# Kernel tuning notes

Hardware: AMD Instinct MI355X
Metric: run time of the kernel (lower is better)

## Reference

```python
import jax, jax.numpy as jnp
import numpy as np
from jax import lax

B, N, F_IN, T = 4, 30000, 2, 12
HID, HORIZON, E = 32, 12, 240000


def setup_inputs() -> dict:
    key = jax.random.key(0)
    ks = jax.random.split(key, 20)

    def lin_init(k, fan_in, shape):
        b = 1.0 / np.sqrt(fan_in)
        return jax.random.uniform(k, shape, jnp.float32, -b, b)

    def glorot(k, shape):
        b = np.sqrt(6.0 / (shape[0] + shape[1]))
        return jax.random.uniform(k, shape, jnp.float32, -b, b)

    return {
        "x": jax.random.normal(ks[0], (B, N, F_IN, T), jnp.float32),
        "edge_index": jax.random.randint(ks[1], (2, E), 0, N, jnp.int32),
        # A3TGCN2 attention over periods (init: uniform[0,1))
        "attention": jax.random.uniform(ks[2], (T,), jnp.float32),
        # TGCN2 gates: GCNConv weight (F_IN,HID) + bias, Linear (2*HID,HID) + bias
        "conv_z_w": glorot(ks[3], (F_IN, HID)), "conv_z_b": jnp.zeros((HID,), jnp.float32),
        "lin_z_w": lin_init(ks[4], 2 * HID, (2 * HID, HID)), "lin_z_b": lin_init(ks[5], 2 * HID, (HID,)),
        "conv_r_w": glorot(ks[6], (F_IN, HID)), "conv_r_b": jnp.zeros((HID,), jnp.float32),
        "lin_r_w": lin_init(ks[7], 2 * HID, (2 * HID, HID)), "lin_r_b": lin_init(ks[8], 2 * HID, (HID,)),
        "conv_h_w": glorot(ks[9], (F_IN, HID)), "conv_h_b": jnp.zeros((HID,), jnp.float32),
        "lin_h_w": lin_init(ks[10], 2 * HID, (2 * HID, HID)), "lin_h_b": lin_init(ks[11], 2 * HID, (HID,)),
        # trailing head Linear(HID, HORIZON)
        "head_w": lin_init(ks[12], HID, (HID, HORIZON)), "head_b": lin_init(ks[13], HID, (HORIZON,)),
    }


def _forward(x, attention, conv_z_w, conv_z_b, lin_z_w, lin_z_b,
             conv_r_w, conv_r_b, lin_r_w, lin_r_b,
             conv_h_w, conv_h_b, lin_h_w, lin_h_b,
             head_w, head_b, edge_index):
    b, n = x.shape[0], x.shape[1]
    # GCN normalization with added self loops: D^-1/2 (A+I) D^-1/2
    loop = jnp.arange(n, dtype=edge_index.dtype)
    src = jnp.concatenate([edge_index[0], loop])  # (E+N,) message sources
    dst = jnp.concatenate([edge_index[1], loop])  # (E+N,) message targets
    deg = jnp.zeros((n,), x.dtype).at[dst].add(1.0)  # deg >= 1 due to self loops
    dinv = lax.rsqrt(deg)
    norm = dinv[src] * dinv[dst]  # (E+N,)

    def gcn(xt, W, bias):
        # xt: (B,N,F) -> (B,N,HID); gather from src, scatter-add to dst
        xw = jnp.einsum('bnf,fh->bnh', xt, W)
        msg = xw[:, src, :] * norm[None, :, None]  # (B,E+N,HID)
        agg = jnp.zeros((b, n, W.shape[1]), xt.dtype).at[:, dst, :].add(msg)
        return agg + bias

    probs = jax.nn.softmax(attention)  # (T,)
    H0 = jnp.zeros((b, n, HID), x.dtype)  # A3TGCN2 passes H=None every period

    def step(acc, inps):
        xt, p = inps  # xt: (B,N,F)
        Z = jax.nn.sigmoid(jnp.concatenate([gcn(xt, conv_z_w, conv_z_b), H0], -1) @ lin_z_w + lin_z_b)
        R = jax.nn.sigmoid(jnp.concatenate([gcn(xt, conv_r_w, conv_r_b), H0], -1) @ lin_r_w + lin_r_b)
        Ht = jnp.tanh(jnp.concatenate([gcn(xt, conv_h_w, conv_h_b), H0 * R], -1) @ lin_h_w + lin_h_b)
        Hn = Z * H0 + (1.0 - Z) * Ht
        return acc + p * Hn, None

    acc, _ = lax.scan(step, H0, (jnp.moveaxis(x, 3, 0), probs))
    return jax.nn.relu(acc) @ head_w + head_b  # (B,N,HORIZON)


def reference(x, edge_index, attention, conv_z_w, conv_z_b, lin_z_w, lin_z_b,
              conv_r_w, conv_r_b, lin_r_w, lin_r_b,
              conv_h_w, conv_h_b, lin_h_w, lin_h_b, head_w, head_b):
    return _forward(x, attention, conv_z_w, conv_z_b, lin_z_w, lin_z_b,
                    conv_r_w, conv_r_b, lin_r_w, lin_r_b,
                    conv_h_w, conv_h_b, lin_h_w, lin_h_b,
                    head_w, head_b, edge_index)
```

## Files before the change

kernel.cpp:

```cpp
#include <hip/hip_runtime.h>

#define BB   4
#define NN   30000
#define TT   12
#define EE   240000
#define FT   24
#define NM   96
#define CAP  32
#define OVCAP 2048
#define FB   ((EE + 255) / 256)
#define LOG2E 1.44269504088896340736f

#define WS_CNT 0
#define WS_OVC 30000
#define WS_EFF 30016
#define WS_OVF 30272
#define WS_BKT 34368

__device__ __forceinline__ float readlane_f(float v, int l) {
    return __int_as_float(__builtin_amdgcn_readlane(__float_as_int(v), l));
}

__global__ void __launch_bounds__(256)
k_pre(const int* __restrict__ src, const int* __restrict__ dst,
      const float* __restrict__ czw, const float* __restrict__ czb,
      const float* __restrict__ lzw, const float* __restrict__ lzb,
      const float* __restrict__ chw, const float* __restrict__ chb,
      const float* __restrict__ lhw, const float* __restrict__ lhb,
      const float* __restrict__ att,
      int* __restrict__ cnt, int* __restrict__ ovc,
      int* __restrict__ ovf, int* __restrict__ bucket, float* __restrict__ eff) {
    int bid = blockIdx.x, lt = threadIdx.x;
    if (bid < FB) {
        int e = bid * 256 + lt;
        if (e < EE) {
            int d = dst[e], s = src[e];
            int slot = atomicAdd(&cnt[d], 1);
            if (slot < CAP) {
                bucket[d * CAP + slot] = s;
            } else {
                int o = atomicAdd(ovc, 1);
                if (o < OVCAP) { ovf[2 * o] = d; ovf[2 * o + 1] = s; }
            }
        }
        return;
    }
    int j = lt;
    if (j < 32) {
        float wz0 = 0.f, wz1 = 0.f, bz = 0.f, wh0 = 0.f, wh1 = 0.f, bh = 0.f;
        for (int k = 0; k < 32; ++k) {
            float lz = lzw[k * 32 + j], lh = lhw[k * 32 + j];
            wz0 = fmaf(czw[k],      lz, wz0);
            wz1 = fmaf(czw[32 + k], lz, wz1);
            bz  = fmaf(czb[k],      lz, bz);
            wh0 = fmaf(chw[k],      lh, wh0);
            wh1 = fmaf(chw[32 + k], lh, wh1);
            bh  = fmaf(chb[k],      lh, bh);
        }
        eff[j]        = -LOG2E * wz0;
        eff[32 + j]   = -LOG2E * wz1;
        eff[64 + j]   = -LOG2E * (bz + lzb[j]);
        eff[96 + j]   = 2.0f * LOG2E * wh0;
        eff[128 + j]  = 2.0f * LOG2E * wh1;
        eff[160 + j]  = 2.0f * LOG2E * (bh + lhb[j]);
    } else if (j == 32) {
        float m = -1e30f;
        for (int t = 0; t < TT; ++t) m = fmaxf(m, att[t]);
        float p[TT], s = 0.f;
        for (int t = 0; t < TT; ++t) { p[t] = __expf(att[t] - m); s += p[t]; }
        float inv = 1.0f / s;
        for (int t = 0; t < TT; ++t) eff[192 + t] = p[t] * inv;
    }
}

__global__ void __launch_bounds__(256)
k_fused(const float* __restrict__ x, const int* __restrict__ cnt,
        const int* __restrict__ ovc, const int* __restrict__ ovf,
        const int* __restrict__ bucket, const float* __restrict__ eff,
        const float* __restrict__ hw, const float* __restrict__ hb,
        float* __restrict__ out) {
    __shared__ float se[204];
    __shared__ float shwT[384];
    __shared__ float shb[12];
    __shared__ float sx[4 * NM];
    __shared__ float lacc[4 * 128];
    const int lt = threadIdx.x, lane = lt & 63, w = lt >> 6;
    const int n = blockIdx.x * 4 + w;

    if (lt < 204) se[lt] = eff[lt];
    if (lt < 12) shb[lt] = hb[lt];
    for (int i = lt; i < 384; i += 256) {
        int jj = i / 12, kk = i - 12 * jj;
        shwT[kk * 32 + jj] = hw[i];
    }
    __syncthreads();

    const bool act = (lane < 48);
    const int b = lane / 12, f2 = lane - 12 * b;
    const float2* xb = (const float2*)x;
    const int lane_off = b * (NN * 12) + f2;

    const int deg = __builtin_amdgcn_readfirstlane(cnt[n]);
    const int m = (deg < CAP) ? deg : CAP;
    int sv = (lane < m) ? bucket[n * CAP + lane] : n;
    float wv = (lane <= m) ? rsqrtf((float)(cnt[sv] + 1)) : 0.f;

    float2 acc = {0.f, 0.f};
    const int total = m + 1;
    int k = 0;
    for (; k + 8 <= total; k += 8) {
        int s0 = __builtin_amdgcn_readlane(sv, k);
        int s1 = __builtin_amdgcn_readlane(sv, k + 1);
        int s2 = __builtin_amdgcn_readlane(sv, k + 2);
        int s3 = __builtin_amdgcn_readlane(sv, k + 3);
        int s4 = __builtin_amdgcn_readlane(sv, k + 4);
        int s5 = __builtin_amdgcn_readlane(sv, k + 5);
        int s6 = __builtin_amdgcn_readlane(sv, k + 6);
        int s7 = __builtin_amdgcn_readlane(sv, k + 7);
        if (act) {
            float2 v0 = xb[lane_off + s0 * 12];
            float2 v1 = xb[lane_off + s1 * 12];
            float2 v2 = xb[lane_off + s2 * 12];
            float2 v3 = xb[lane_off + s3 * 12];
            float2 v4 = xb[lane_off + s4 * 12];
            float2 v5 = xb[lane_off + s5 * 12];
            float2 v6 = xb[lane_off + s6 * 12];
            float2 v7 = xb[lane_off + s7 * 12];
            float w0 = readlane_f(wv, k),     w1 = readlane_f(wv, k + 1);
            float w2 = readlane_f(wv, k + 2), w3 = readlane_f(wv, k + 3);
            float w4 = readlane_f(wv, k + 4), w5 = readlane_f(wv, k + 5);
            float w6 = readlane_f(wv, k + 6), w7 = readlane_f(wv, k + 7);
            acc.x = fmaf(w0, v0.x, acc.x); acc.y = fmaf(w0, v0.y, acc.y);
            acc.x = fmaf(w1, v1.x, acc.x); acc.y = fmaf(w1, v1.y, acc.y);
            acc.x = fmaf(w2, v2.x, acc.x); acc.y = fmaf(w2, v2.y, acc.y);
            acc.x = fmaf(w3, v3.x, acc.x); acc.y = fmaf(w3, v3.y, acc.y);
            acc.x = fmaf(w4, v4.x, acc.x); acc.y = fmaf(w4, v4.y, acc.y);
            acc.x = fmaf(w5, v5.x, acc.x); acc.y = fmaf(w5, v5.y, acc.y);
            acc.x = fmaf(w6, v6.x, acc.x); acc.y = fmaf(w6, v6.y, acc.y);
            acc.x = fmaf(w7, v7.x, acc.x); acc.y = fmaf(w7, v7.y, acc.y);
        }
    }
    for (; k < total; k += 4) {
        int s0 = __builtin_amdgcn_readlane(sv, k);
        int s1 = __builtin_amdgcn_readlane(sv, k + 1);
        int s2 = __builtin_amdgcn_readlane(sv, k + 2);
        int s3 = __builtin_amdgcn_readlane(sv, k + 3);
        if (act) {
            float2 v0 = xb[lane_off + s0 * 12];
            float2 v1 = xb[lane_off + s1 * 12];
            float2 v2 = xb[lane_off + s2 * 12];
            float2 v3 = xb[lane_off + s3 * 12];
            float w0 = readlane_f(wv, k),     w1 = readlane_f(wv, k + 1);
            float w2 = readlane_f(wv, k + 2), w3 = readlane_f(wv, k + 3);
            acc.x = fmaf(w0, v0.x, acc.x); acc.y = fmaf(w0, v0.y, acc.y);
            acc.x = fmaf(w1, v1.x, acc.x); acc.y = fmaf(w1, v1.y, acc.y);
            acc.x = fmaf(w2, v2.x, acc.x); acc.y = fmaf(w2, v2.y, acc.y);
            acc.x = fmaf(w3, v3.x, acc.x); acc.y = fmaf(w3, v3.y, acc.y);
        }
    }

    int nov = __builtin_amdgcn_readfirstlane(*ovc);
    if (nov > 0) {
        if (nov > OVCAP) nov = OVCAP;
        for (int i = 0; i < nov; ++i) {
            int d = ovf[2 * i];
            if (d == n) {
                int s = ovf[2 * i + 1];
                float ws_ = rsqrtf((float)(cnt[s] + 1));
                if (act) {
                    float2 v = xb[lane_off + s * 12];
                    acc.x = fmaf(ws_, v.x, acc.x);
                    acc.y = fmaf(ws_, v.y, acc.y);
                }
            }
        }
    }

    const float dn = readlane_f(wv, m);
    if (act) {
        float2* sx2 = (float2*)(sx + w * NM + b * FT);
        sx2[f2] = make_float2(dn * acc.x, dn * acc.y);
    }
    __syncthreads();

    const int j = lane & 31, b0_ = lane >> 5;
    const float az0 = se[j],      az1 = se[32 + j],  ab = se[64 + j];
    const float ch0 = se[96 + j], ch1 = se[128 + j], cb = se[160 + j];
#pragma unroll
    for (int bi = 0; bi < 2; ++bi) {
        const int bb = b0_ + 2 * bi;
        const float4* s4 = (const float4*)(sx + w * NM + bb * FT);
        float4 q[6];
#pragma unroll
        for (int i = 0; i < 6; ++i) q[i] = s4[i];
        const float* av = (const float*)q;
        float a = 0.f;
#pragma unroll
        for (int t = 0; t < TT; ++t) {
            float v0 = av[t], v1 = av[12 + t], pp = se[192 + t];
            float ae = fmaf(v1, az1, fmaf(v0, az0, ab));
            float ce = fmaf(v1, ch1, fmaf(v0, ch0, cb));
            ae = __builtin_amdgcn_fmed3f(ae, -126.f, 126.f);
            ce = __builtin_amdgcn_fmed3f(ce, -126.f, 126.f);
            float u  = __builtin_amdgcn_exp2f(ae);
            float e2 = __builtin_amdgcn_exp2f(ce);
            float t1  = 1.0f + u;
            float den = fmaf(e2, t1, t1);
            float num = fmaf(u, e2, -u);
            float r   = __builtin_amdgcn_rcpf(den);
            a = fmaf(pp * num, r, a);
        }
        lacc[w * 128 + bb * 32 + j] = fmaxf(a, 0.f);
    }
    __syncthreads();

    if (lane < 48) {
        int bb = lane / 12, kk = lane - 12 * bb;
        float r = shb[kk];
        const float4* la4 = (const float4*)(lacc + w * 128 + bb * 32);
        const float4* wt4 = (const float4*)(shwT + kk * 32);
#pragma unroll
        for (int i = 0; i < 8; ++i) {
            float4 a4 = la4[i], w4 = wt4[i];
            r = fmaf(a4.x, w4.x, r); r = fmaf(a4.y, w4.y, r);
            r = fmaf(a4.z, w4.z, r); r = fmaf(a4.w, w4.w, r);
        }
        out[((long long)bb * NN + n) * 12 + kk] = r;
    }
}

extern "C" void kernel_launch(void* const* d_in, const int* in_sizes, int n_in,
                              void* d_out, int out_size, void* d_ws, size_t ws_size,
                              hipStream_t stream) {
    const float* x   = (const float*)d_in[0];
    const int*   ei  = (const int*)d_in[1];
    const float* att = (const float*)d_in[2];
    const float* czw = (const float*)d_in[3];
    const float* czb = (const float*)d_in[4];
    const float* lzw = (const float*)d_in[5];
    const float* lzb = (const float*)d_in[6];
    const float* chw = (const float*)d_in[11];
    const float* chb = (const float*)d_in[12];
    const float* lhw = (const float*)d_in[13];
    const float* lhb = (const float*)d_in[14];
    const float* hw  = (const float*)d_in[15];
    const float* hb  = (const float*)d_in[16];
    float* out = (float*)d_out;

    float* ws = (float*)d_ws;
    int*   cnt = (int*)(ws + WS_CNT);
    int*   ovc = (int*)(ws + WS_OVC);
    float* eff = ws + WS_EFF;
    int*   ovf = (int*)(ws + WS_OVF);
    int*   bkt = (int*)(ws + WS_BKT);

    const int* src = ei;
    const int* dst = ei + EE;

    hipMemsetAsync(cnt, 0, WS_EFF * 4, stream);
    k_pre<<<FB + 1, 256, 0, stream>>>(src, dst, czw, czb, lzw, lzb,
                                      chw, chb, lhw, lhb, att,
                                      cnt, ovc, ovf, bkt, eff);
    k_fused<<<NN / 4, 256, 0, stream>>>(x, cnt, ovc, ovf, bkt, eff, hw, hb, out);
}
```

Before: 141.9 us.

## Process two nodes per wavefront with interleaved gathers and wave-level barriers

Each wavefront now handles two destination nodes, interleaving their 8-wide neighbor gathers so more independent global loads are in flight per wave. The block-wide __syncthreads are replaced by wave barriers, since each wave only touches its own shared-memory slices. Shared-memory rows are padded to a stride of 36 to reduce bank conflicts, and the grid is halved. The trade-offs are higher register pressure, fewer blocks, and the remainder loop now always issues full 8-wide gathers, reading padded lanes that carry zero weight.

```diff
diff --git a/kernel.cpp b/kernel.cpp
--- a/kernel.cpp
+++ b/kernel.cpp
@@ -73,6 +73,41 @@
     }
 }
 
+__device__ __forceinline__ void gath8(const float2* __restrict__ xb, int lane_off,
+                                      bool act, int sv, float wv, int k,
+                                      float2& acc) {
+    int s0 = __builtin_amdgcn_readlane(sv, k);
+    int s1 = __builtin_amdgcn_readlane(sv, k + 1);
+    int s2 = __builtin_amdgcn_readlane(sv, k + 2);
+    int s3 = __builtin_amdgcn_readlane(sv, k + 3);
+    int s4 = __builtin_amdgcn_readlane(sv, k + 4);
+    int s5 = __builtin_amdgcn_readlane(sv, k + 5);
+    int s6 = __builtin_amdgcn_readlane(sv, k + 6);
+    int s7 = __builtin_amdgcn_readlane(sv, k + 7);
+    if (act) {
+        float2 v0 = xb[lane_off + s0 * 12];
+        float2 v1 = xb[lane_off + s1 * 12];
+        float2 v2 = xb[lane_off + s2 * 12];
+        float2 v3 = xb[lane_off + s3 * 12];
+        float2 v4 = xb[lane_off + s4 * 12];
+        float2 v5 = xb[lane_off + s5 * 12];
+        float2 v6 = xb[lane_off + s6 * 12];
+        float2 v7 = xb[lane_off + s7 * 12];
+        float w0 = readlane_f(wv, k),     w1 = readlane_f(wv, k + 1);
+        float w2 = readlane_f(wv, k + 2), w3 = readlane_f(wv, k + 3);
+        float w4 = readlane_f(wv, k + 4), w5 = readlane_f(wv, k + 5);
+        float w6 = readlane_f(wv, k + 6), w7 = readlane_f(wv, k + 7);
+        acc.x = fmaf(w0, v0.x, acc.x); acc.y = fmaf(w0, v0.y, acc.y);
+        acc.x = fmaf(w1, v1.x, acc.x); acc.y = fmaf(w1, v1.y, acc.y);
+        acc.x = fmaf(w2, v2.x, acc.x); acc.y = fmaf(w2, v2.y, acc.y);
+        acc.x = fmaf(w3, v3.x, acc.x); acc.y = fmaf(w3, v3.y, acc.y);
+        acc.x = fmaf(w4, v4.x, acc.x); acc.y = fmaf(w4, v4.y, acc.y);
+        acc.x = fmaf(w5, v5.x, acc.x); acc.y = fmaf(w5, v5.y, acc.y);
+        acc.x = fmaf(w6, v6.x, acc.x); acc.y = fmaf(w6, v6.y, acc.y);
+        acc.x = fmaf(w7, v7.x, acc.x); acc.y = fmaf(w7, v7.y, acc.y);
+    }
+}
+
 __global__ void __launch_bounds__(256)
 k_fused(const float* __restrict__ x, const int* __restrict__ cnt,
         const int* __restrict__ ovc, const int* __restrict__ ovf,
@@ -80,18 +115,19 @@
         const float* __restrict__ hw, const float* __restrict__ hb,
         float* __restrict__ out) {
     __shared__ float se[204];
-    __shared__ float shwT[384];
+    __shared__ float shwT[432];
     __shared__ float shb[12];
-    __shared__ float sx[4 * NM];
-    __shared__ float lacc[4 * 128];
+    __shared__ float sx[8 * NM];
+    __shared__ float lacc[32 * 36];
     const int lt = threadIdx.x, lane = lt & 63, w = lt >> 6;
-    const int n = blockIdx.x * 4 + w;
+    const int n0 = blockIdx.x * 8 + w * 2;
+    const int n1 = n0 + 1;
 
     if (lt < 204) se[lt] = eff[lt];
     if (lt < 12) shb[lt] = hb[lt];
     for (int i = lt; i < 384; i += 256) {
         int jj = i / 12, kk = i - 12 * jj;
-        shwT[kk * 32 + jj] = hw[i];
+        shwT[kk * 36 + jj] = hw[i];
     }
     __syncthreads();
 
@@ -100,63 +136,21 @@
     const float2* xb = (const float2*)x;
     const int lane_off = b * (NN * 12) + f2;
 
-    const int deg = __builtin_amdgcn_readfirstlane(cnt[n]);
-    const int m = (deg < CAP) ? deg : CAP;
-    int sv = (lane < m) ? bucket[n * CAP + lane] : n;
-    float wv = (lane <= m) ? rsqrtf((float)(cnt[sv] + 1)) : 0.f;
-
-    float2 acc = {0.f, 0.f};
-    const int total = m + 1;
-    int k = 0;
-    for (; k + 8 <= total; k += 8) {
-        int s0 = __builtin_amdgcn_readlane(sv, k);
-        int s1 = __builtin_amdgcn_readlane(sv, k + 1);
-        int s2 = __builtin_amdgcn_readlane(sv, k + 2);
-        int s3 = __builtin_amdgcn_readlane(sv, k + 3);
-        int s4 = __builtin_amdgcn_readlane(sv, k + 4);
-        int s5 = __builtin_amdgcn_readlane(sv, k + 5);
-        int s6 = __builtin_amdgcn_readlane(sv, k + 6);
-        int s7 = __builtin_amdgcn_readlane(sv, k + 7);
-        if (act) {
-            float2 v0 = xb[lane_off + s0 * 12];
-            float2 v1 = xb[lane_off + s1 * 12];
-            float2 v2 = xb[lane_off + s2 * 12];
-            float2 v3 = xb[lane_off + s3 * 12];
-            float2 v4 = xb[lane_off + s4 * 12];
-            float2 v5 = xb[lane_off + s5 * 12];
-            float2 v6 = xb[lane_off + s6 * 12];
-            float2 v7 = xb[lane_off + s7 * 12];
-            float w0 = readlane_f(wv, k),     w1 = readlane_f(wv, k + 1);
-            float w2 = readlane_f(wv, k + 2), w3 = readlane_f(wv, k + 3);
-            float w4 = readlane_f(wv, k + 4), w5 = readlane_f(wv, k + 5);
-            float w6 = readlane_f(wv, k + 6), w7 = readlane_f(wv, k + 7);
-            acc.x = fmaf(w0, v0.x, acc.x); acc.y = fmaf(w0, v0.y, acc.y);
-            acc.x = fmaf(w1, v1.x, acc.x); acc.y = fmaf(w1, v1.y, acc.y);
-            acc.x = fmaf(w2, v2.x, acc.x); acc.y = fmaf(w2, v2.y, acc.y);
-            acc.x = fmaf(w3, v3.x, acc.x); acc.y = fmaf(w3, v3.y, acc.y);
-            acc.x = fmaf(w4, v4.x, acc.x); acc.y = fmaf(w4, v4.y, acc.y);
-            acc.x = fmaf(w5, v5.x, acc.x); acc.y = fmaf(w5, v5.y, acc.y);
-            acc.x = fmaf(w6, v6.x, acc.x); acc.y = fmaf(w6, v6.y, acc.y);
-            acc.x = fmaf(w7, v7.x, acc.x); acc.y = fmaf(w7, v7.y, acc.y);
-        }
-    }
-    for (; k < total; k += 4) {
-        int s0 = __builtin_amdgcn_readlane(sv, k);
-        int s1 = __builtin_amdgcn_readlane(sv, k + 1);
-        int s2 = __builtin_amdgcn_readlane(sv, k + 2);
-        int s3 = __builtin_amdgcn_readlane(sv, k + 3);
-        if (act) {
-            float2 v0 = xb[lane_off + s0 * 12];
-            float2 v1 = xb[lane_off + s1 * 12];
-            float2 v2 = xb[lane_off + s2 * 12];
-            float2 v3 = xb[lane_off + s3 * 12];
-            float w0 = readlane_f(wv, k),     w1 = readlane_f(wv, k + 1);
-            float w2 = readlane_f(wv, k + 2), w3 = readlane_f(wv, k + 3);
-            acc.x = fmaf(w0, v0.x, acc.x); acc.y = fmaf(w0, v0.y, acc.y);
-            acc.x = fmaf(w1, v1.x, acc.x); acc.y = fmaf(w1, v1.y, acc.y);
-            acc.x = fmaf(w2, v2.x, acc.x); acc.y = fmaf(w2, v2.y, acc.y);
-            acc.x = fmaf(w3, v3.x, acc.x); acc.y = fmaf(w3, v3.y, acc.y);
-        }
+    const int deg0 = __builtin_amdgcn_readfirstlane(cnt[n0]);
+    const int deg1 = __builtin_amdgcn_readfirstlane(cnt[n1]);
+    const int m0 = (deg0 < CAP) ? deg0 : CAP;
+    const int m1 = (deg1 < CAP) ? deg1 : CAP;
+    int sv0 = (lane < m0) ? bucket[n0 * CAP + lane] : n0;
+    int sv1 = (lane < m1) ? bucket[n1 * CAP + lane] : n1;
+    float wv0 = (lane <= m0) ? rsqrtf((float)(cnt[sv0] + 1)) : 0.f;
+    float wv1 = (lane <= m1) ? rsqrtf((float)(cnt[sv1] + 1)) : 0.f;
+
+    float2 acc0 = {0.f, 0.f}, acc1 = {0.f, 0.f};
+    const int t0 = m0 + 1, t1 = m1 + 1;
+    const int tmax = (t0 > t1) ? t0 : t1;
+    for (int k = 0; k < tmax; k += 8) {
+        if (k < t0) gath8(xb, lane_off, act, sv0, wv0, k, acc0);
+        if (k < t1) gath8(xb, lane_off, act, sv1, wv1, k, acc1);
     }
 
     int nov = __builtin_amdgcn_readfirstlane(*ovc);
@@ -164,68 +158,77 @@
         if (nov > OVCAP) nov = OVCAP;
         for (int i = 0; i < nov; ++i) {
             int d = ovf[2 * i];
-            if (d == n) {
+            if (d == n0 || d == n1) {
                 int s = ovf[2 * i + 1];
                 float ws_ = rsqrtf((float)(cnt[s] + 1));
                 if (act) {
                     float2 v = xb[lane_off + s * 12];
-                    acc.x = fmaf(ws_, v.x, acc.x);
-                    acc.y = fmaf(ws_, v.y, acc.y);
+                    if (d == n0) { acc0.x = fmaf(ws_, v.x, acc0.x); acc0.y = fmaf(ws_, v.y, acc0.y); }
+                    else         { acc1.x = fmaf(ws_, v.x, acc1.x); acc1.y = fmaf(ws_, v.y, acc1.y); }
                 }
             }
         }
     }
 
-    const float dn = readlane_f(wv, m);
+    const float dn0 = readlane_f(wv0, m0);
+    const float dn1 = readlane_f(wv1, m1);
     if (act) {
-        float2* sx2 = (float2*)(sx + w * NM + b * FT);
-        sx2[f2] = make_float2(dn * acc.x, dn * acc.y);
-    }
-    __syncthreads();
+        float2* p0 = (float2*)(sx + (w * 2) * NM + b * FT);
+        p0[f2] = make_float2(dn0 * acc0.x, dn0 * acc0.y);
+        float2* p1 = (float2*)(sx + (w * 2 + 1) * NM + b * FT);
+        p1[f2] = make_float2(dn1 * acc1.x, dn1 * acc1.y);
+    }
+    __builtin_amdgcn_wave_barrier();
 
     const int j = lane & 31, b0_ = lane >> 5;
     const float az0 = se[j],      az1 = se[32 + j],  ab = se[64 + j];
     const float ch0 = se[96 + j], ch1 = se[128 + j], cb = se[160 + j];
 #pragma unroll
-    for (int bi = 0; bi < 2; ++bi) {
-        const int bb = b0_ + 2 * bi;
-        const float4* s4 = (const float4*)(sx + w * NM + bb * FT);
-        float4 q[6];
-#pragma unroll
-        for (int i = 0; i < 6; ++i) q[i] = s4[i];
-        const float* av = (const float*)q;
-        float a = 0.f;
-#pragma unroll
-        for (int t = 0; t < TT; ++t) {
-            float v0 = av[t], v1 = av[12 + t], pp = se[192 + t];
-            float ae = fmaf(v1, az1, fmaf(v0, az0, ab));
-            float ce = fmaf(v1, ch1, fmaf(v0, ch0, cb));
-            ae = __builtin_amdgcn_fmed3f(ae, -126.f, 126.f);
-            ce = __builtin_amdgcn_fmed3f(ce, -126.f, 126.f);
-            float u  = __builtin_amdgcn_exp2f(ae);
-            float e2 = __builtin_amdgcn_exp2f(ce);
-            float t1  = 1.0f + u;
-            float den = fmaf(e2, t1, t1);
-            float num = fmaf(u, e2, -u);
-            float r   = __builtin_amdgcn_rcpf(den);
-            a = fmaf(pp * num, r, a);
-        }
-        lacc[w * 128 + bb * 32 + j] = fmaxf(a, 0.f);
-    }
-    __syncthreads();
+    for (int nd = 0; nd < 2; ++nd) {
+#pragma unroll
+        for (int bi = 0; bi < 2; ++bi) {
+            const int bb = b0_ + 2 * bi;
+            const float4* s4 = (const float4*)(sx + (w * 2 + nd) * NM + bb * FT);
+            float4 q[6];
+#pragma unroll
+            for (int i = 0; i < 6; ++i) q[i] = s4[i];
+            const float* av = (const float*)q;
+            float a = 0.f;
+#pragma unroll
+            for (int t = 0; t < TT; ++t) {
+                float v0 = av[t], v1 = av[12 + t], pp = se[192 + t];
+                float ae = fmaf(v1, az1, fmaf(v0, az0, ab));
+                float ce = fmaf(v1, ch1, fmaf(v0, ch0, cb));
+                ae = __builtin_amdgcn_fmed3f(ae, -126.f, 126.f);
+                ce = __builtin_amdgcn_fmed3f(ce, -126.f, 126.f);
+                float u  = __builtin_amdgcn_exp2f(ae);
+                float e2 = __builtin_amdgcn_exp2f(ce);
+                float t1_ = 1.0f + u;
+                float den = fmaf(e2, t1_, t1_);
+                float num = fmaf(u, e2, -u);
+                float r   = __builtin_amdgcn_rcpf(den);
+                a = fmaf(pp * num, r, a);
+            }
+            lacc[((w * 2 + nd) * 4 + bb) * 36 + j] = fmaxf(a, 0.f);
+        }
+    }
+    __builtin_amdgcn_wave_barrier();
 
     if (lane < 48) {
         int bb = lane / 12, kk = lane - 12 * bb;
-        float r = shb[kk];
-        const float4* la4 = (const float4*)(lacc + w * 128 + bb * 32);
-        const float4* wt4 = (const float4*)(shwT + kk * 32);
-#pragma unroll
-        for (int i = 0; i < 8; ++i) {
-            float4 a4 = la4[i], w4 = wt4[i];
-            r = fmaf(a4.x, w4.x, r); r = fmaf(a4.y, w4.y, r);
-            r = fmaf(a4.z, w4.z, r); r = fmaf(a4.w, w4.w, r);
-        }
-        out[((long long)bb * NN + n) * 12 + kk] = r;
+        const float4* wt4 = (const float4*)(shwT + kk * 36);
+#pragma unroll
+        for (int nd = 0; nd < 2; ++nd) {
+            float r = shb[kk];
+            const float4* la4 = (const float4*)(lacc + ((w * 2 + nd) * 4 + bb) * 36);
+#pragma unroll
+            for (int i = 0; i < 8; ++i) {
+                float4 a4 = la4[i], w4 = wt4[i];
+                r = fmaf(a4.x, w4.x, r); r = fmaf(a4.y, w4.y, r);
+                r = fmaf(a4.z, w4.z, r); r = fmaf(a4.w, w4.w, r);
+            }
+            out[((long long)bb * NN + (n0 + nd)) * 12 + kk] = r;
+        }
     }
 }
 
@@ -261,5 +264,5 @@
     k_pre<<<FB + 1, 256, 0, stream>>>(src, dst, czw, czb, lzw, lzb,
                                       chw, chb, lhw, lhb, att,
                                       cnt, ovc, ovf, bkt, eff);
-    k_fused<<<NN / 4, 256, 0, stream>>>(x, cnt, ovc, ovf, bkt, eff, hw, hb, out);
-}
+    k_fused<<<NN / 8, 256, 0, stream>>>(x, cnt, ovc, ovf, bkt, eff, hw, hb, out);
+}
```

After: 148.4 us. 4.5% more time.
